# Performance work log

Hardware: AMD Instinct MI355X
Metric: run time of the kernel (lower is better)

The kernel has to match this reference:

```python
import math
import jax, jax.numpy as jnp
import numpy as np

K = 1.0            # Lorentz manifold curvature k
B, S = 4, 2048     # batch, seq_len
IN, H, OUT = 512, 8, 64   # in_channels, num_heads, out_channels (space dim; head_dim = OUT+1)


def setup_inputs() -> dict:
    key = jax.random.key(0)
    ks = jax.random.split(key, 8)
    std = 1.0 / math.sqrt(IN)
    return {
        "query_input": jax.random.normal(ks[0], (B, S, IN), jnp.float32),
        "source_input": jax.random.normal(ks[1], (B, S, IN), jnp.float32),
        # per-head HypLinear weights stacked on a leading head axis: [H, OUT, IN]
        "Wq_w": jax.random.normal(ks[2], (H, OUT, IN), jnp.float32) * std,
        "Wq_b": jnp.zeros((H, OUT), jnp.float32),
        "Wk_w": jax.random.normal(ks[3], (H, OUT, IN), jnp.float32) * std,
        "Wk_b": jnp.zeros((H, OUT), jnp.float32),
        "Wv_w": jax.random.normal(ks[4], (H, OUT, IN), jnp.float32) * std,
        "Wv_b": jnp.zeros((H, OUT), jnp.float32),
        "scale": jnp.array([math.sqrt(OUT)], jnp.float32),  # nn.Parameter([sqrt(out_channels)])
        "bias": jnp.zeros((), jnp.float32),                 # nn.Parameter(zeros(()))
    }


def hyp_linear(x, w, b):
    # HypLinear: linear map to space part, recompute Lorentz time coord sqrt(||x_s||^2 + k)
    sp = jnp.einsum('bsi,hoi->bsho', x, w) + b            # [B,S,H,OUT]
    t = jnp.sqrt(jnp.sum(sp * sp, axis=-1, keepdims=True) + K)
    return jnp.concatenate([t, sp], axis=-1)              # [B,S,H,OUT+1]


def reference(query_input, source_input, Wq_w, Wq_b, Wk_w, Wk_b, Wv_w, Wv_b, scale, bias):
    q = hyp_linear(query_input, Wq_w, Wq_b)   # [B,S,H,D], D = OUT+1
    k = hyp_linear(source_input, Wk_w, Wk_b)
    v = hyp_linear(source_input, Wv_w, Wv_b)

    # Lorentzian cinner: <x,y>_L = -x0*y0 + <x_s, y_s>
    sgn = jnp.concatenate([-jnp.ones((1,), q.dtype), jnp.ones((OUT,), q.dtype)])
    att = jnp.einsum('bqhd,bkhd->bhqk', q * sgn, k)       # [B,H,S,S]
    att = (2.0 + 2.0 * att) / scale[0] + bias

    causal = jnp.triu(jnp.full((S, S), -1e9, q.dtype), 1)  # causal mask (additive)
    att = jax.nn.softmax(att + causal, axis=-1)

    ctx = jnp.einsum('bhqk,bkhd->bqhd', att, v)           # [B,S,H,D]

    # manifold.mid_point over the heads axis (dim=-2)
    ave = jnp.mean(ctx, axis=2)                           # [B,S,D]
    inner = -ave[..., :1] ** 2 + jnp.sum(ave[..., 1:] ** 2, axis=-1, keepdims=True)
    denom = jnp.sqrt(jnp.maximum(jnp.abs(-inner), 1e-8))
    return math.sqrt(K) * ave / denom                     # [B,S,D]
```

## Files before the change

### kernel.cpp

```cpp
#include <hip/hip_runtime.h>

#define BATCH 4
#define SEQ   2048
#define INC   512
#define NH    8
#define OUTC  64
#define DD    65

typedef float f32x4 __attribute__((ext_vector_type(4)));
typedef short short8 __attribute__((ext_vector_type(8)));

static __device__ __forceinline__ unsigned short f2b(float f) {
  unsigned int u = __float_as_uint(f);
  u = (u + 0x7FFFu + ((u >> 16) & 1u)) >> 16;
  return (unsigned short)u;
}

static __device__ __forceinline__ unsigned int pk2(float lo, float hi) {
  unsigned int r;
  asm("v_cvt_pk_bf16_f32 %0, %1, %2" : "=v"(r) : "v"(lo), "v"(hi));
  return r;
}

#define GLDS(g, l) __builtin_amdgcn_global_load_lds( \
    (const __attribute__((address_space(1))) void*)(g), \
    (__attribute__((address_space(3))) void*)(l), 16, 0, 0)

__global__ __launch_bounds__(256) void proj_kernel(
    const float* __restrict__ Xq, const float* __restrict__ Xs,
    const float* __restrict__ Wq, const float* __restrict__ Wqb,
    const float* __restrict__ Wk, const float* __restrict__ Wkb,
    const float* __restrict__ Wv, const float* __restrict__ Wvb,
    unsigned short* __restrict__ qs, float* __restrict__ qt,
    unsigned short* __restrict__ ks, float* __restrict__ kt,
    unsigned short* __restrict__ vs, float* __restrict__ vt)
{
  const int which = blockIdx.z;
  const float* X  = (which == 0) ? Xq : Xs;
  const float* W  = (which == 0) ? Wq : (which == 1 ? Wk : Wv);
  const float* Bb = (which == 0) ? Wqb : (which == 1 ? Wkb : Wvb);
  unsigned short* outs = (which == 0) ? qs : (which == 1 ? ks : vs);
  float* outt = (which == 0) ? qt : (which == 1 ? kt : vt);

  const int m0 = blockIdx.x * 64;
  const int h  = blockIdx.y;
  const int n0 = h * 64;

  __shared__ alignas(16) unsigned short lX[64 * 64];
  __shared__ alignas(16) unsigned short lW[64 * 64];

  const int tid  = threadIdx.x;
  const int lane = tid & 63;
  const int wave = tid >> 6;
  const int arow = lane & 15;
  const int agrp = lane >> 4;

  f32x4 acc[4] = {};

  for (int k0 = 0; k0 < INC; k0 += 64) {
    __syncthreads();
#pragma unroll
    for (int u0 = 0; u0 < 2; ++u0) {
      int u = tid + u0 * 256;
      int row = u >> 3, ch = u & 7;
      int slot = ch ^ (row & 7);
      {
        const f32x4* src = (const f32x4*)(X + (size_t)(m0 + row) * INC + k0 + ch * 8);
        f32x4 a = src[0], b = src[1];
        short8 p;
        p[0]=f2b(a[0]); p[1]=f2b(a[1]); p[2]=f2b(a[2]); p[3]=f2b(a[3]);
        p[4]=f2b(b[0]); p[5]=f2b(b[1]); p[6]=f2b(b[2]); p[7]=f2b(b[3]);
        *(short8*)&lX[row * 64 + slot * 8] = p;
      }
      {
        const f32x4* src = (const f32x4*)(W + (size_t)(n0 + row) * INC + k0 + ch * 8);
        f32x4 a = src[0], b = src[1];
        short8 p;
        p[0]=f2b(a[0]); p[1]=f2b(a[1]); p[2]=f2b(a[2]); p[3]=f2b(a[3]);
        p[4]=f2b(b[0]); p[5]=f2b(b[1]); p[6]=f2b(b[2]); p[7]=f2b(b[3]);
        *(short8*)&lW[row * 64 + slot * 8] = p;
      }
    }
    __syncthreads();
#pragma unroll
    for (int kc = 0; kc < 2; ++kc) {
      short8 af = *(const short8*)&lX[(wave * 16 + arow) * 64 + (((kc * 4 + agrp) ^ (arow & 7)) * 8)];
#pragma unroll
      for (int c = 0; c < 4; ++c) {
        short8 bf = *(const short8*)&lW[(c * 16 + arow) * 64 + (((kc * 4 + agrp) ^ (arow & 7)) * 8)];
        acc[c] = __builtin_amdgcn_mfma_f32_16x16x32_bf16(af, bf, acc[c], 0, 0, 0);
      }
    }
  }

  float bcol[4];
#pragma unroll
  for (int c = 0; c < 4; ++c) bcol[c] = Bb[n0 + c * 16 + arow];
#pragma unroll
  for (int r = 0; r < 4; ++r) {
    float s2 = 0.f;
#pragma unroll
    for (int c = 0; c < 4; ++c) {
      float v = acc[c][r] + bcol[c];
      acc[c][r] = v;
      s2 += v * v;
    }
    s2 += __shfl_xor(s2, 1); s2 += __shfl_xor(s2, 2);
    s2 += __shfl_xor(s2, 4); s2 += __shfl_xor(s2, 8);
    float tv = sqrtf(s2 + 1.0f);
    int gs = m0 + wave * 16 + agrp * 4 + r;
    int bi = gs >> 11, si = gs & (SEQ - 1);
    size_t rowbase = (size_t)(bi * NH + h) * SEQ + si;
    size_t obase = rowbase * 64;
#pragma unroll
    for (int c = 0; c < 4; ++c) outs[obase + c * 16 + arow] = f2b(acc[c][r]);
    if (arow == 0) outt[rowbase] = tv;
  }
}

__global__ __launch_bounds__(256) void transpose_v_kernel(
    const unsigned short* __restrict__ vs, unsigned short* __restrict__ vT)
{
  const int bh = blockIdx.y;
  const int s0 = blockIdx.x * 64;
  __shared__ unsigned short lT[64 * 80];
  const int tid = threadIdx.x;
#pragma unroll
  for (int u0 = 0; u0 < 2; ++u0) {
    int u = tid + u0 * 256;
    int row = u >> 3, ch = u & 7;
    short8 v = *(const short8*)&vs[((size_t)bh * SEQ + s0 + row) * 64 + ch * 8];
    *(short8*)&lT[row * 80 + ch * 8] = v;
  }
  __syncthreads();
#pragma unroll
  for (int u0 = 0; u0 < 2; ++u0) {
    int u = tid + u0 * 256;
    int o = u >> 3, sc = u & 7;
    short8 w;
#pragma unroll
    for (int j = 0; j < 8; ++j) w[j] = lT[(sc * 8 + j) * 80 + o];
    *(short8*)&vT[((size_t)bh * 64 + o) * SEQ + s0 + sc * 8] = w;
  }
}

__device__ __forceinline__ void stage_kv(
    const unsigned short* kgp, const unsigned short* vgp,
    unsigned short* dK, unsigned short* dV,
    int k0, int wave, int rl, int chx)
{
  const int r0 = wave * 8 + rl;
  const int r1 = r0 + 32;
  GLDS(kgp + (size_t)(k0 + r0) * 64 + chx, dK + wave * 512);
  GLDS(kgp + (size_t)(k0 + r1) * 64 + chx, dK + 2048 + wave * 512);
  GLDS(vgp + (size_t)r0 * SEQ + k0 + chx, dV + wave * 512);
  GLDS(vgp + (size_t)r1 * SEQ + k0 + chx, dV + 2048 + wave * 512);
}

__global__ __launch_bounds__(256) void attn_kernel(
    const unsigned short* __restrict__ qs, const float* __restrict__ qt,
    const unsigned short* __restrict__ ks, const float* __restrict__ ktm,
    const unsigned short* __restrict__ vT, const float* __restrict__ vtm,
    const float* __restrict__ scale_p, float* __restrict__ ctx)
{
  const int xb = blockIdx.x;
  const int bh = blockIdx.y;
  const float a = 2.0f / scale_p[0];

  __shared__ alignas(16) unsigned short lK[2][64 * 64];
  __shared__ alignas(16) unsigned short lV[2][64 * 64];
  __shared__ alignas(16) unsigned short lP[4][16 * 128];
  __shared__ alignas(16) float lkt[SEQ];
  __shared__ alignas(16) float lvt[SEQ];

  const int tid  = threadIdx.x;
  const int lane = tid & 63;
  const int wave = tid >> 6;
  const int arow = lane & 15;
  const int agrp = lane >> 4;

  const size_t bhbase = (size_t)bh * SEQ;
  const unsigned short* kgp = ks + bhbase * 64;
  const unsigned short* vgp = vT + (size_t)bh * 64 * SEQ;

  const int rl  = lane >> 3;
  const int chx = ((lane & 7) ^ rl) * 8;
  const int dsl0 = (agrp ^ (arow & 7)) * 8;
  const int dsl1 = ((4 + agrp) ^ (arow & 7)) * 8;
  const int swE  = (arow & 15) << 3;
  unsigned short* myP = &lP[wave][0];

  for (int pp = 0; pp < 2; ++pp) {
    const int qb = pp ? (31 - xb) : xb;
    const int q0 = qb * 64;
    const int wq = wave * 16 + arow;

    const unsigned short* qp = qs + (bhbase + q0 + wq) * 64;
    short8 qf0 = *(const short8*)(qp + agrp * 8);
    short8 qf1 = *(const short8*)(qp + 32 + agrp * 8);
    const float aqt = a * qt[bhbase + q0 + wq];

#pragma unroll
    for (int i = 0; i < 2; ++i) {
      *(f32x4*)&lkt[tid * 8 + i * 4] = *(const f32x4*)&ktm[bhbase + tid * 8 + i * 4];
      *(f32x4*)&lvt[tid * 8 + i * 4] = *(const f32x4*)&vtm[bhbase + tid * 8 + i * 4];
    }
    stage_kv(kgp, vgp, lK[0], lV[0], 0, wave, rl, chx);
    asm volatile("s_waitcnt lgkmcnt(0)");

    float m_ = -1e30f, lsum = 0.f, ctxt = 0.f;
    f32x4 acc[4] = {};

    for (int kti = 0; kti <= qb; ++kti) {
      const int cur = kti & 1;
      const int k0 = kti * 64;
      if (kti < qb) {
        stage_kv(kgp, vgp, lK[cur ^ 1], lV[cur ^ 1], k0 + 64, wave, rl, chx);
        asm volatile("s_waitcnt vmcnt(4)");
      } else {
        asm volatile("s_waitcnt vmcnt(0)");
      }
      __builtin_amdgcn_s_barrier();

      const unsigned short* Kb = lK[cur];
      const unsigned short* Vb = lV[cur];

      f32x4 sS[4] = {};
      __builtin_amdgcn_s_setprio(1);
#pragma unroll
      for (int c = 0; c < 4; ++c) {
        short8 kf = *(const short8*)&Kb[(c * 16 + arow) * 64 + dsl0];
        sS[c] = __builtin_amdgcn_mfma_f32_16x16x32_bf16(kf, qf0, sS[c], 0, 0, 0);
      }
#pragma unroll
      for (int c = 0; c < 4; ++c) {
        short8 kf = *(const short8*)&Kb[(c * 16 + arow) * 64 + dsl1];
        sS[c] = __builtin_amdgcn_mfma_f32_16x16x32_bf16(kf, qf1, sS[c], 0, 0, 0);
      }
      __builtin_amdgcn_s_setprio(0);

#pragma unroll
      for (int c = 0; c < 4; ++c) {
        f32x4 kv = *(const f32x4*)&lkt[k0 + c * 16 + agrp * 4];
#pragma unroll
        for (int r = 0; r < 4; ++r)
          sS[c][r] = fmaf(a, sS[c][r], -(aqt * kv[r]));
      }
      if (kti == qb) {
#pragma unroll
        for (int c = 0; c < 4; ++c)
#pragma unroll
          for (int r = 0; r < 4; ++r)
            if (c * 16 + agrp * 4 + r > wq) sS[c][r] = -1e30f;
      }

      float mx0 = fmaxf(fmaxf(sS[0][0], sS[0][1]), fmaxf(sS[0][2], sS[0][3]));
      float mx1 = fmaxf(fmaxf(sS[1][0], sS[1][1]), fmaxf(sS[1][2], sS[1][3]));
      float mx2 = fmaxf(fmaxf(sS[2][0], sS[2][1]), fmaxf(sS[2][2], sS[2][3]));
      float mx3 = fmaxf(fmaxf(sS[3][0], sS[3][1]), fmaxf(sS[3][2], sS[3][3]));
      float mx = fmaxf(fmaxf(mx0, mx1), fmaxf(mx2, mx3));
      mx = fmaxf(mx, __shfl_xor(mx, 16));
      mx = fmaxf(mx, __shfl_xor(mx, 32));
      float mn = fmaxf(m_, mx);
      float fac = __expf(m_ - mn);
      m_ = mn;

      float psum = 0.f, cpart = 0.f;
#pragma unroll
      for (int c = 0; c < 4; ++c) {
        f32x4 vv = *(const f32x4*)&lvt[k0 + c * 16 + agrp * 4];
#pragma unroll
        for (int r = 0; r < 4; ++r) {
          float p = __expf(sS[c][r] - m_);
          sS[c][r] = p;
          psum += p;
          cpart = fmaf(p, vv[r], cpart);
        }
      }
      lsum = lsum * fac + psum;
      ctxt = ctxt * fac + cpart;

#pragma unroll
      for (int r = 0; r < 4; ++r) {
        float facr = __shfl(fac, agrp * 4 + r);
        acc[0][r] *= facr; acc[1][r] *= facr;
        acc[2][r] *= facr; acc[3][r] *= facr;
      }

#pragma unroll
      for (int c = 0; c < 4; ++c) {
        unsigned int w0 = pk2(sS[c][0], sS[c][1]);
        unsigned int w1 = pk2(sS[c][2], sS[c][3]);
        *(unsigned int*)&myP[arow * 128 + ((c * 16 + agrp * 4) ^ swE)]     = w0;
        *(unsigned int*)&myP[arow * 128 + ((c * 16 + agrp * 4 + 2) ^ swE)] = w1;
      }

      __builtin_amdgcn_s_setprio(1);
#pragma unroll
      for (int kc = 0; kc < 2; ++kc) {
        short8 pf = *(const short8*)&myP[arow * 128 + ((kc * 32 + agrp * 8) ^ swE)];
        const int dsl = kc ? dsl1 : dsl0;
#pragma unroll
        for (int dc = 0; dc < 4; ++dc) {
          short8 vf = *(const short8*)&Vb[(dc * 16 + arow) * 64 + dsl];
          acc[dc] = __builtin_amdgcn_mfma_f32_16x16x32_bf16(pf, vf, acc[dc], 0, 0, 0);
        }
      }
      __builtin_amdgcn_s_setprio(0);

      __builtin_amdgcn_s_barrier();
    }

    float lsum_t = lsum + __shfl_xor(lsum, 16);
    lsum_t += __shfl_xor(lsum_t, 32);
    float ctxt_t = ctxt + __shfl_xor(ctxt, 16);
    ctxt_t += __shfl_xor(ctxt_t, 32);
    float inv = 1.0f / lsum_t;
    if (agrp == 0)
      ctx[(bhbase + q0 + wave * 16 + arow) * (size_t)DD] = ctxt_t * inv;
#pragma unroll
    for (int r = 0; r < 4; ++r) {
      float invr = __shfl(inv, agrp * 4 + r);
      size_t rb = (bhbase + q0 + wave * 16 + agrp * 4 + r) * (size_t)DD;
#pragma unroll
      for (int dc = 0; dc < 4; ++dc)
        ctx[rb + 1 + dc * 16 + arow] = acc[dc][r] * invr;
    }
  }
}

__global__ __launch_bounds__(256) void finalize_kernel(
    const float* __restrict__ ctx, float* __restrict__ out)
{
  const int tid  = threadIdx.x;
  const int lane = tid & 63;
  const int gw = blockIdx.x * 4 + (tid >> 6);
  const int b = gw >> 11, si = gw & (SEQ - 1);
  float v = 0.f, v64 = 0.f;
#pragma unroll
  for (int h = 0; h < NH; ++h) {
    size_t base = ((size_t)(b * NH + h) * SEQ + si) * (size_t)DD;
    v += ctx[base + lane];
    if (lane == 0) v64 += ctx[base + 64];
  }
  float ave   = v * 0.125f;
  float ave64 = v64 * 0.125f;
  float contrib = (lane == 0) ? (ave64 * ave64 - ave * ave) : ave * ave;
  contrib += __shfl_xor(contrib, 1);
  contrib += __shfl_xor(contrib, 2);
  contrib += __shfl_xor(contrib, 4);
  contrib += __shfl_xor(contrib, 8);
  contrib += __shfl_xor(contrib, 16);
  contrib += __shfl_xor(contrib, 32);
  float denom = sqrtf(fmaxf(fabsf(contrib), 1e-8f));
  size_t ob = ((size_t)b * SEQ + si) * (size_t)DD;
  out[ob + lane] = ave / denom;
  if (lane == 0) out[ob + 64] = ave64 / denom;
}

extern "C" void kernel_launch(void* const* d_in, const int* in_sizes, int n_in,
                              void* d_out, int out_size, void* d_ws, size_t ws_size,
                              hipStream_t stream) {
  const float* Xq  = (const float*)d_in[0];
  const float* Xs  = (const float*)d_in[1];
  const float* Wq  = (const float*)d_in[2];
  const float* Wqb = (const float*)d_in[3];
  const float* Wk  = (const float*)d_in[4];
  const float* Wkb = (const float*)d_in[5];
  const float* Wv  = (const float*)d_in[6];
  const float* Wvb = (const float*)d_in[7];
  const float* scale = (const float*)d_in[8];
  float* out = (float*)d_out;

  char* ws = (char*)d_ws;
  const size_t NROW = (size_t)BATCH * NH * SEQ;
  unsigned short* qsb = (unsigned short*)ws; ws += NROW * 64 * 2;
  unsigned short* ksb = (unsigned short*)ws; ws += NROW * 64 * 2;
  unsigned short* vsb = (unsigned short*)ws; ws += NROW * 64 * 2;
  unsigned short* vTb = (unsigned short*)ws; ws += NROW * 64 * 2;
  float* qtb = (float*)ws; ws += NROW * 4;
  float* ktb = (float*)ws; ws += NROW * 4;
  float* vtb = (float*)ws; ws += NROW * 4;
  float* ctx = (float*)ws; ws += NROW * (size_t)DD * 4;

  proj_kernel<<<dim3(128, NH, 3), 256, 0, stream>>>(
      Xq, Xs, Wq, Wqb, Wk, Wkb, Wv, Wvb, qsb, qtb, ksb, ktb, vsb, vtb);
  transpose_v_kernel<<<dim3(SEQ / 64, BATCH * NH), 256, 0, stream>>>(vsb, vTb);
  attn_kernel<<<dim3(16, BATCH * NH), 256, 0, stream>>>(
      qsb, qtb, ksb, ktb, vTb, vtb, scale, ctx);
  finalize_kernel<<<(BATCH * SEQ) / 4, 256, 0, stream>>>(ctx, out);
}
```

Baseline: 113.4 us.

## Pre-convert inputs to bf16, pipeline projection, fold time coords into MFMA

Adds a separate bf16 conversion kernel so the projection GEMM can stage operands with async global-to-LDS loads and double buffering. In attention, the Lorentz time-coordinate terms and the softmax row sum are folded into extra MFMA calls, using hi/lo bf16 splits and a ones column, instead of scalar FMAs reading LDS tables. Blocks are remapped per XCD, exp uses exp2 with a pre-folded log2e, and the P buffer shrinks. This costs an extra kernel pass and traffic over the inputs, plus extra MFMAs with some bf16 precision risk.

```diff
diff --git a/kernel.cpp b/kernel.cpp
--- a/kernel.cpp
+++ b/kernel.cpp
@@ -9,13 +9,18 @@
 
 typedef float f32x4 __attribute__((ext_vector_type(4)));
 typedef short short8 __attribute__((ext_vector_type(8)));
-
-static __device__ __forceinline__ unsigned short f2b(float f) {
+typedef short short4v __attribute__((ext_vector_type(4)));
+typedef unsigned int uint2v __attribute__((ext_vector_type(2)));
+typedef unsigned short us;
+
+static __device__ __forceinline__ us f2b(float f) {
   unsigned int u = __float_as_uint(f);
   u = (u + 0x7FFFu + ((u >> 16) & 1u)) >> 16;
-  return (unsigned short)u;
-}
-
+  return (us)u;
+}
+static __device__ __forceinline__ float b2f(us h) {
+  return __uint_as_float(((unsigned int)h) << 16);
+}
 static __device__ __forceinline__ unsigned int pk2(float lo, float hi) {
   unsigned int r;
   asm("v_cvt_pk_bf16_f32 %0, %1, %2" : "=v"(r) : "v"(lo), "v"(hi));
@@ -26,71 +31,94 @@
     (const __attribute__((address_space(1))) void*)(g), \
     (__attribute__((address_space(3))) void*)(l), 16, 0, 0)
 
+__global__ __launch_bounds__(256) void tobf16_kernel(
+    const float* __restrict__ Xq, const float* __restrict__ Xs,
+    const float* __restrict__ Wq, const float* __restrict__ Wk,
+    const float* __restrict__ Wv,
+    us* __restrict__ dXq, us* __restrict__ dXs,
+    us* __restrict__ dWq, us* __restrict__ dWk, us* __restrict__ dWv)
+{
+  const int which = blockIdx.y;
+  const float* src;
+  us* dst;
+  int n;
+  switch (which) {
+    case 0: src = Xq; dst = dXq; n = BATCH * SEQ * INC; break;
+    case 1: src = Xs; dst = dXs; n = BATCH * SEQ * INC; break;
+    case 2: src = Wq; dst = dWq; n = NH * OUTC * INC; break;
+    case 3: src = Wk; dst = dWk; n = NH * OUTC * INC; break;
+    default: src = Wv; dst = dWv; n = NH * OUTC * INC; break;
+  }
+  for (long i = (long)blockIdx.x * 256 + threadIdx.x; i * 4 < n;
+       i += (long)gridDim.x * 256) {
+    f32x4 v = *(const f32x4*)(src + i * 4);
+    short4v o;
+    o[0] = (short)f2b(v[0]); o[1] = (short)f2b(v[1]);
+    o[2] = (short)f2b(v[2]); o[3] = (short)f2b(v[3]);
+    *(short4v*)(dst + i * 4) = o;
+  }
+}
+
 __global__ __launch_bounds__(256) void proj_kernel(
-    const float* __restrict__ Xq, const float* __restrict__ Xs,
-    const float* __restrict__ Wq, const float* __restrict__ Wqb,
-    const float* __restrict__ Wk, const float* __restrict__ Wkb,
-    const float* __restrict__ Wv, const float* __restrict__ Wvb,
-    unsigned short* __restrict__ qs, float* __restrict__ qt,
-    unsigned short* __restrict__ ks, float* __restrict__ kt,
-    unsigned short* __restrict__ vs, float* __restrict__ vt)
+    const us* __restrict__ Xqb, const us* __restrict__ Xsb,
+    const us* __restrict__ Wqb, const us* __restrict__ Wkb, const us* __restrict__ Wvb,
+    const float* __restrict__ Bq, const float* __restrict__ Bk, const float* __restrict__ Bv,
+    us* __restrict__ qs, float* __restrict__ qt,
+    us* __restrict__ ks, us* __restrict__ kta,
+    us* __restrict__ vs, us* __restrict__ vth, us* __restrict__ vtl)
 {
   const int which = blockIdx.z;
-  const float* X  = (which == 0) ? Xq : Xs;
-  const float* W  = (which == 0) ? Wq : (which == 1 ? Wk : Wv);
-  const float* Bb = (which == 0) ? Wqb : (which == 1 ? Wkb : Wvb);
-  unsigned short* outs = (which == 0) ? qs : (which == 1 ? ks : vs);
-  float* outt = (which == 0) ? qt : (which == 1 ? kt : vt);
+  const us* X = (which == 0) ? Xqb : Xsb;
+  const us* W = (which == 0) ? Wqb : (which == 1 ? Wkb : Wvb);
+  const float* Bb = (which == 0) ? Bq : (which == 1 ? Bk : Bv);
+  us* outs = (which == 0) ? qs : (which == 1 ? ks : vs);
 
   const int m0 = blockIdx.x * 64;
   const int h  = blockIdx.y;
   const int n0 = h * 64;
 
-  __shared__ alignas(16) unsigned short lX[64 * 64];
-  __shared__ alignas(16) unsigned short lW[64 * 64];
+  __shared__ alignas(16) us lX[2][64 * 64];
+  __shared__ alignas(16) us lW[2][64 * 64];
 
   const int tid  = threadIdx.x;
   const int lane = tid & 63;
   const int wave = tid >> 6;
   const int arow = lane & 15;
   const int agrp = lane >> 4;
+  const int rl   = lane >> 3;
+  const int chx  = ((lane & 7) ^ rl) * 8;
+  const int r0   = wave * 8 + rl;
+  const int r1   = r0 + 32;
+
+#define PSTAGE(buf, k0) do { \
+    GLDS(X + (size_t)(m0 + r0) * INC + (k0) + chx, &lX[buf][wave * 512]); \
+    GLDS(X + (size_t)(m0 + r1) * INC + (k0) + chx, &lX[buf][2048 + wave * 512]); \
+    GLDS(W + (size_t)(n0 + r0) * INC + (k0) + chx, &lW[buf][wave * 512]); \
+    GLDS(W + (size_t)(n0 + r1) * INC + (k0) + chx, &lW[buf][2048 + wave * 512]); \
+  } while (0)
 
   f32x4 acc[4] = {};
-
-  for (int k0 = 0; k0 < INC; k0 += 64) {
-    __syncthreads();
-#pragma unroll
-    for (int u0 = 0; u0 < 2; ++u0) {
-      int u = tid + u0 * 256;
-      int row = u >> 3, ch = u & 7;
-      int slot = ch ^ (row & 7);
-      {
-        const f32x4* src = (const f32x4*)(X + (size_t)(m0 + row) * INC + k0 + ch * 8);
-        f32x4 a = src[0], b = src[1];
-        short8 p;
-        p[0]=f2b(a[0]); p[1]=f2b(a[1]); p[2]=f2b(a[2]); p[3]=f2b(a[3]);
-        p[4]=f2b(b[0]); p[5]=f2b(b[1]); p[6]=f2b(b[2]); p[7]=f2b(b[3]);
-        *(short8*)&lX[row * 64 + slot * 8] = p;
-      }
-      {
-        const f32x4* src = (const f32x4*)(W + (size_t)(n0 + row) * INC + k0 + ch * 8);
-        f32x4 a = src[0], b = src[1];
-        short8 p;
-        p[0]=f2b(a[0]); p[1]=f2b(a[1]); p[2]=f2b(a[2]); p[3]=f2b(a[3]);
-        p[4]=f2b(b[0]); p[5]=f2b(b[1]); p[6]=f2b(b[2]); p[7]=f2b(b[3]);
-        *(short8*)&lW[row * 64 + slot * 8] = p;
-      }
-    }
-    __syncthreads();
+  PSTAGE(0, 0);
+
+  for (int kk = 0; kk < 8; ++kk) {
+    const int cur = kk & 1;
+    if (kk < 7) {
+      PSTAGE(cur ^ 1, (kk + 1) * 64);
+      asm volatile("s_waitcnt vmcnt(4)");
+    } else {
+      asm volatile("s_waitcnt vmcnt(0)");
+    }
+    __builtin_amdgcn_s_barrier();
 #pragma unroll
     for (int kc = 0; kc < 2; ++kc) {
-      short8 af = *(const short8*)&lX[(wave * 16 + arow) * 64 + (((kc * 4 + agrp) ^ (arow & 7)) * 8)];
+      short8 af = *(const short8*)&lX[cur][(wave * 16 + arow) * 64 + (((kc * 4 + agrp) ^ (arow & 7)) * 8)];
 #pragma unroll
       for (int c = 0; c < 4; ++c) {
-        short8 bf = *(const short8*)&lW[(c * 16 + arow) * 64 + (((kc * 4 + agrp) ^ (arow & 7)) * 8)];
+        short8 bf = *(const short8*)&lW[cur][(c * 16 + arow) * 64 + (((kc * 4 + agrp) ^ (arow & 7)) * 8)];
         acc[c] = __builtin_amdgcn_mfma_f32_16x16x32_bf16(af, bf, acc[c], 0, 0, 0);
       }
     }
+    __builtin_amdgcn_s_barrier();
   }
 
   float bcol[4];
@@ -114,16 +142,33 @@
     size_t obase = rowbase * 64;
 #pragma unroll
     for (int c = 0; c < 4; ++c) outs[obase + c * 16 + arow] = f2b(acc[c][r]);
-    if (arow == 0) outt[rowbase] = tv;
+    if (arow == 0) {
+      if (which == 0) {
+        qt[rowbase] = tv;
+      } else {
+        us th = f2b(tv);
+        us tl = f2b(tv - b2f(th));
+        if (which == 1) {
+          short8 row = {};
+          row[0] = (short)(th ^ 0x8000);
+          row[1] = (short)(tl ^ 0x8000);
+          row[2] = (short)(th ^ 0x8000);
+          *(short8*)&kta[rowbase * 8] = row;
+        } else {
+          vth[rowbase] = th;
+          vtl[rowbase] = tl;
+        }
+      }
+    }
   }
 }
 
 __global__ __launch_bounds__(256) void transpose_v_kernel(
-    const unsigned short* __restrict__ vs, unsigned short* __restrict__ vT)
+    const us* __restrict__ vs, us* __restrict__ vT)
 {
   const int bh = blockIdx.y;
   const int s0 = blockIdx.x * 64;
-  __shared__ unsigned short lT[64 * 80];
+  __shared__ us lT[64 * 80];
   const int tid = threadIdx.x;
 #pragma unroll
   for (int u0 = 0; u0 < 2; ++u0) {
@@ -144,34 +189,23 @@
   }
 }
 
-__device__ __forceinline__ void stage_kv(
-    const unsigned short* kgp, const unsigned short* vgp,
-    unsigned short* dK, unsigned short* dV,
-    int k0, int wave, int rl, int chx)
-{
-  const int r0 = wave * 8 + rl;
-  const int r1 = r0 + 32;
-  GLDS(kgp + (size_t)(k0 + r0) * 64 + chx, dK + wave * 512);
-  GLDS(kgp + (size_t)(k0 + r1) * 64 + chx, dK + 2048 + wave * 512);
-  GLDS(vgp + (size_t)r0 * SEQ + k0 + chx, dV + wave * 512);
-  GLDS(vgp + (size_t)r1 * SEQ + k0 + chx, dV + 2048 + wave * 512);
-}
-
 __global__ __launch_bounds__(256) void attn_kernel(
-    const unsigned short* __restrict__ qs, const float* __restrict__ qt,
-    const unsigned short* __restrict__ ks, const float* __restrict__ ktm,
-    const unsigned short* __restrict__ vT, const float* __restrict__ vtm,
+    const us* __restrict__ qs, const float* __restrict__ qt,
+    const us* __restrict__ ks, const us* __restrict__ kta,
+    const us* __restrict__ vT, const us* __restrict__ vth, const us* __restrict__ vtl,
     const float* __restrict__ scale_p, float* __restrict__ ctx)
 {
-  const int xb = blockIdx.x;
-  const int bh = blockIdx.y;
-  const float a = 2.0f / scale_p[0];
-
-  __shared__ alignas(16) unsigned short lK[2][64 * 64];
-  __shared__ alignas(16) unsigned short lV[2][64 * 64];
-  __shared__ alignas(16) unsigned short lP[4][16 * 128];
-  __shared__ alignas(16) float lkt[SEQ];
-  __shared__ alignas(16) float lvt[SEQ];
+  const int f = blockIdx.x + 16 * blockIdx.y;
+  const int xcd = f & 7, slot = f >> 3;
+  const int bh = xcd * 4 + (slot >> 4);
+  const int xb = slot & 15;
+  const float al2 = (2.0f / scale_p[0]) * 1.44269504088896f;
+
+  __shared__ alignas(16) us lK[2][64 * 64];
+  __shared__ alignas(16) us lV[2][64 * 64];
+  __shared__ alignas(16) us lKt[2][64 * 8];
+  __shared__ alignas(16) us lVt[2][512];
+  __shared__ alignas(16) us lP[4][16 * 64];
 
   const int tid  = threadIdx.x;
   const int lane = tid & 63;
@@ -180,50 +214,69 @@
   const int agrp = lane >> 4;
 
   const size_t bhbase = (size_t)bh * SEQ;
-  const unsigned short* kgp = ks + bhbase * 64;
-  const unsigned short* vgp = vT + (size_t)bh * 64 * SEQ;
-
-  const int rl  = lane >> 3;
-  const int chx = ((lane & 7) ^ rl) * 8;
+  const us* kgp  = ks  + bhbase * 64;
+  const us* vgp  = vT  + (size_t)bh * 64 * SEQ;
+  const us* ktg  = kta + bhbase * 8;
+  const us* vthg = vth + bhbase;
+  const us* vtlg = vtl + bhbase;
+
+  const int rl   = lane >> 3;
+  const int chx  = ((lane & 7) ^ rl) * 8;
+  const int r0s  = wave * 8 + rl;
+  const int r1s  = r0s + 32;
   const int dsl0 = (agrp ^ (arow & 7)) * 8;
   const int dsl1 = ((4 + agrp) ^ (arow & 7)) * 8;
-  const int swE  = (arow & 15) << 3;
-  unsigned short* myP = &lP[wave][0];
+  const int swE  = (arow & 7) * 8;
+  us* myP = &lP[wave][0];
+
+  const us* vtsrc = (((lane >> 3) & 1) ? vtlg : vthg) + (lane & 7) * 8;
+
+#define ASTAGE(buf, k0) do { \
+    GLDS(kgp + (size_t)((k0) + r0s) * 64 + chx, &lK[buf][wave * 512]); \
+    GLDS(kgp + (size_t)((k0) + r1s) * 64 + chx, &lK[buf][2048 + wave * 512]); \
+    GLDS(vgp + (size_t)r0s * SEQ + (k0) + chx, &lV[buf][wave * 512]); \
+    GLDS(vgp + (size_t)r1s * SEQ + (k0) + chx, &lV[buf][2048 + wave * 512]); \
+    GLDS(ktg + (size_t)((k0) + lane) * 8, &lKt[buf][0]); \
+    GLDS(vtsrc + (k0), &lVt[buf][0]); \
+  } while (0)
+
+  short8 ones8;
+#pragma unroll
+  for (int j = 0; j < 8; ++j) ones8[j] = (short)0x3F80;
 
   for (int pp = 0; pp < 2; ++pp) {
     const int qb = pp ? (31 - xb) : xb;
     const int q0 = qb * 64;
     const int wq = wave * 16 + arow;
 
-    const unsigned short* qp = qs + (bhbase + q0 + wq) * 64;
+    ASTAGE(0, 0);
+
+    const us* qp = qs + (bhbase + q0 + wq) * 64;
     short8 qf0 = *(const short8*)(qp + agrp * 8);
     short8 qf1 = *(const short8*)(qp + 32 + agrp * 8);
-    const float aqt = a * qt[bhbase + q0 + wq];
-
-#pragma unroll
-    for (int i = 0; i < 2; ++i) {
-      *(f32x4*)&lkt[tid * 8 + i * 4] = *(const f32x4*)&ktm[bhbase + tid * 8 + i * 4];
-      *(f32x4*)&lvt[tid * 8 + i * 4] = *(const f32x4*)&vtm[bhbase + tid * 8 + i * 4];
-    }
-    stage_kv(kgp, vgp, lK[0], lV[0], 0, wave, rl, chx);
-    asm volatile("s_waitcnt lgkmcnt(0)");
-
-    float m_ = -1e30f, lsum = 0.f, ctxt = 0.f;
-    f32x4 acc[4] = {};
+    float qtv = qt[bhbase + q0 + wq];
+    us qh = f2b(qtv);
+    us ql = f2b(qtv - b2f(qh));
+    short8 qf2 = {};
+    if (agrp == 0) { qf2[0] = (short)qh; qf2[1] = (short)qh; qf2[2] = (short)ql; }
+
+    float m_ = -1e30f;
+    f32x4 acc[5] = {};
 
     for (int kti = 0; kti <= qb; ++kti) {
       const int cur = kti & 1;
-      const int k0 = kti * 64;
       if (kti < qb) {
-        stage_kv(kgp, vgp, lK[cur ^ 1], lV[cur ^ 1], k0 + 64, wave, rl, chx);
-        asm volatile("s_waitcnt vmcnt(4)");
+        ASTAGE(cur ^ 1, (kti + 1) * 64);
+        asm volatile("s_waitcnt vmcnt(6)");
       } else {
         asm volatile("s_waitcnt vmcnt(0)");
       }
       __builtin_amdgcn_s_barrier();
 
-      const unsigned short* Kb = lK[cur];
-      const unsigned short* Vb = lV[cur];
+      const us* Kb  = lK[cur];
+      const us* Vb  = lV[cur];
+      const us* Ktb = lKt[cur];
+      const us* Vtb = lVt[cur];
 
       f32x4 sS[4] = {};
       __builtin_amdgcn_s_setprio(1);
@@ -237,15 +290,14 @@
         short8 kf = *(const short8*)&Kb[(c * 16 + arow) * 64 + dsl1];
         sS[c] = __builtin_amdgcn_mfma_f32_16x16x32_bf16(kf, qf1, sS[c], 0, 0, 0);
       }
+#pragma unroll
+      for (int c = 0; c < 4; ++c) {
+        short8 kf2 = {};
+        if (agrp == 0) kf2 = *(const short8*)&Ktb[(c * 16 + arow) * 8];
+        sS[c] = __builtin_amdgcn_mfma_f32_16x16x32_bf16(kf2, qf2, sS[c], 0, 0, 0);
+      }
       __builtin_amdgcn_s_setprio(0);
 
-#pragma unroll
-      for (int c = 0; c < 4; ++c) {
-        f32x4 kv = *(const f32x4*)&lkt[k0 + c * 16 + agrp * 4];
-#pragma unroll
-        for (int r = 0; r < 4; ++r)
-          sS[c][r] = fmaf(a, sS[c][r], -(aqt * kv[r]));
-      }
       if (kti == qb) {
 #pragma unroll
         for (int c = 0; c < 4; ++c)
@@ -262,66 +314,59 @@
       mx = fmaxf(mx, __shfl_xor(mx, 16));
       mx = fmaxf(mx, __shfl_xor(mx, 32));
       float mn = fmaxf(m_, mx);
-      float fac = __expf(m_ - mn);
+      float fac = exp2f(al2 * (m_ - mn));
       m_ = mn;
-
-      float psum = 0.f, cpart = 0.f;
-#pragma unroll
-      for (int c = 0; c < 4; ++c) {
-        f32x4 vv = *(const f32x4*)&lvt[k0 + c * 16 + agrp * 4];
-#pragma unroll
-        for (int r = 0; r < 4; ++r) {
-          float p = __expf(sS[c][r] - m_);
-          sS[c][r] = p;
-          psum += p;
-          cpart = fmaf(p, vv[r], cpart);
-        }
-      }
-      lsum = lsum * fac + psum;
-      ctxt = ctxt * fac + cpart;
+      float almn = al2 * mn;
+
+#pragma unroll
+      for (int c = 0; c < 4; ++c)
+#pragma unroll
+        for (int r = 0; r < 4; ++r)
+          sS[c][r] = exp2f(fmaf(al2, sS[c][r], -almn));
 
 #pragma unroll
       for (int r = 0; r < 4; ++r) {
         float facr = __shfl(fac, agrp * 4 + r);
-        acc[0][r] *= facr; acc[1][r] *= facr;
-        acc[2][r] *= facr; acc[3][r] *= facr;
+        acc[0][r] *= facr; acc[1][r] *= facr; acc[2][r] *= facr;
+        acc[3][r] *= facr; acc[4][r] *= facr;
       }
 
 #pragma unroll
       for (int c = 0; c < 4; ++c) {
-        unsigned int w0 = pk2(sS[c][0], sS[c][1]);
-        unsigned int w1 = pk2(sS[c][2], sS[c][3]);
-        *(unsigned int*)&myP[arow * 128 + ((c * 16 + agrp * 4) ^ swE)]     = w0;
-        *(unsigned int*)&myP[arow * 128 + ((c * 16 + agrp * 4 + 2) ^ swE)] = w1;
+        uint2v w;
+        w[0] = pk2(sS[c][0], sS[c][1]);
+        w[1] = pk2(sS[c][2], sS[c][3]);
+        *(uint2v*)&myP[arow * 64 + ((c * 16 + agrp * 4) ^ swE)] = w;
       }
 
       __builtin_amdgcn_s_setprio(1);
 #pragma unroll
       for (int kc = 0; kc < 2; ++kc) {
-        short8 pf = *(const short8*)&myP[arow * 128 + ((kc * 32 + agrp * 8) ^ swE)];
+        short8 pf = *(const short8*)&myP[arow * 64 + ((kc * 32 + agrp * 8) ^ swE)];
         const int dsl = kc ? dsl1 : dsl0;
 #pragma unroll
         for (int dc = 0; dc < 4; ++dc) {
           short8 vf = *(const short8*)&Vb[(dc * 16 + arow) * 64 + dsl];
           acc[dc] = __builtin_amdgcn_mfma_f32_16x16x32_bf16(pf, vf, acc[dc], 0, 0, 0);
         }
+        short8 vf4 = {};
+        if (arow < 2)  vf4 = *(const short8*)&Vtb[arow * 64 + kc * 32 + agrp * 8];
+        if (arow == 2) vf4 = ones8;
+        acc[4] = __builtin_amdgcn_mfma_f32_16x16x32_bf16(pf, vf4, acc[4], 0, 0, 0);
       }
       __builtin_amdgcn_s_setprio(0);
 
       __builtin_amdgcn_s_barrier();
     }
 
-    float lsum_t = lsum + __shfl_xor(lsum, 16);
-    lsum_t += __shfl_xor(lsum_t, 32);
-    float ctxt_t = ctxt + __shfl_xor(ctxt, 16);
-    ctxt_t += __shfl_xor(ctxt_t, 32);
-    float inv = 1.0f / lsum_t;
-    if (agrp == 0)
-      ctx[(bhbase + q0 + wave * 16 + arow) * (size_t)DD] = ctxt_t * inv;
 #pragma unroll
     for (int r = 0; r < 4; ++r) {
-      float invr = __shfl(inv, agrp * 4 + r);
+      float ls = __shfl(acc[4][r], (agrp << 4) | 2);
+      float t0 = __shfl(acc[4][r], (agrp << 4) | 0);
+      float t1 = __shfl(acc[4][r], (agrp << 4) | 1);
+      float invr = 1.0f / ls;
       size_t rb = (bhbase + q0 + wave * 16 + agrp * 4 + r) * (size_t)DD;
+      if (arow == 0) ctx[rb] = (t0 + t1) * invr;
 #pragma unroll
       for (int dc = 0; dc < 4; ++dc)
         ctx[rb + 1 + dc * 16 + arow] = acc[dc][r] * invr;
@@ -364,29 +409,40 @@
   const float* Xq  = (const float*)d_in[0];
   const float* Xs  = (const float*)d_in[1];
   const float* Wq  = (const float*)d_in[2];
-  const float* Wqb = (const float*)d_in[3];
+  const float* Bq  = (const float*)d_in[3];
   const float* Wk  = (const float*)d_in[4];
-  const float* Wkb = (const float*)d_in[5];
+  const float* Bk  = (const float*)d_in[5];
   const float* Wv  = (const float*)d_in[6];
-  const float* Wvb = (const float*)d_in[7];
+  const float* Bv  = (const float*)d_in[7];
   const float* scale = (const float*)d_in[8];
   float* out = (float*)d_out;
 
-  char* ws = (char*)d_ws;
+  char* p = (char*)d_ws;
   const size_t NROW = (size_t)BATCH * NH * SEQ;
-  unsigned short* qsb = (unsigned short*)ws; ws += NROW * 64 * 2;
-  unsigned short* ksb = (unsigned short*)ws; ws += NROW * 64 * 2;
-  unsigned short* vsb = (unsigned short*)ws; ws += NROW * 64 * 2;
-  unsigned short* vTb = (unsigned short*)ws; ws += NROW * 64 * 2;
-  float* qtb = (float*)ws; ws += NROW * 4;
-  float* ktb = (float*)ws; ws += NROW * 4;
-  float* vtb = (float*)ws; ws += NROW * 4;
-  float* ctx = (float*)ws; ws += NROW * (size_t)DD * 4;
-
+
+  float* ctx = (float*)p;
+  us* Xqb = (us*)p;
+  us* Xsb = (us*)(p + 8388608);
+  p += 17040128;
+  us* Wqb16 = (us*)p; p += 524288;
+  us* Wkb16 = (us*)p; p += 524288;
+  us* Wvb16 = (us*)p; p += 524288;
+  us* qsb = (us*)p; p += NROW * 64 * 2;
+  us* ksb = (us*)p; p += NROW * 64 * 2;
+  us* vsb = (us*)p; p += NROW * 64 * 2;
+  us* vTb = (us*)p; p += NROW * 64 * 2;
+  float* qtb = (float*)p; p += NROW * 4;
+  us* ktaw = (us*)p; p += NROW * 8 * 2;
+  us* vthw = (us*)p; p += NROW * 2;
+  us* vtlw = (us*)p; p += NROW * 2;
+
+  tobf16_kernel<<<dim3(1024, 5), 256, 0, stream>>>(
+      Xq, Xs, Wq, Wk, Wv, Xqb, Xsb, Wqb16, Wkb16, Wvb16);
   proj_kernel<<<dim3(128, NH, 3), 256, 0, stream>>>(
-      Xq, Xs, Wq, Wqb, Wk, Wkb, Wv, Wvb, qsb, qtb, ksb, ktb, vsb, vtb);
+      Xqb, Xsb, Wqb16, Wkb16, Wvb16, Bq, Bk, Bv,
+      qsb, qtb, ksb, ktaw, vsb, vthw, vtlw);
   transpose_v_kernel<<<dim3(SEQ / 64, BATCH * NH), 256, 0, stream>>>(vsb, vTb);
   attn_kernel<<<dim3(16, BATCH * NH), 256, 0, stream>>>(
-      qsb, qtb, ksb, ktb, vTb, vtb, scale, ctx);
+      qsb, qtb, ksb, ktaw, vTb, vthw, vtlw, scale, ctx);
   finalize_kernel<<<(BATCH * SEQ) / 4, 256, 0, stream>>>(ctx, out);
 }
```

Result: no change. 111.8 us (-1.4%).
